# Kernel optimization log

Hardware: AMD Instinct MI355X
Metric: run time of the kernel (lower is better)

## Reference

```python
import jax, jax.numpy as jnp
import numpy as np

N = 100000   # nodes
E = 1600000  # edges (before self loops)
IN, HID, OUT = 128, 128, 64


def setup_inputs() -> dict:
    key = jax.random.key(0)
    ks = jax.random.split(key, 5)
    x = jax.random.normal(ks[0], (N, IN), dtype=jnp.float32)
    edge_index = jax.random.randint(ks[1], (2, E), 0, N, dtype=jnp.int32)
    W1 = jax.random.normal(ks[2], (IN, HID), dtype=jnp.float32) * (1.0 / np.sqrt(IN))
    b1 = jnp.zeros((HID,), dtype=jnp.float32)
    W2 = jax.random.normal(ks[3], (HID, OUT), dtype=jnp.float32) * (1.0 / np.sqrt(HID))
    b2 = jnp.zeros((OUT,), dtype=jnp.float32)
    return {"x": x, "edge_index": edge_index, "W1": W1, "b1": b1, "W2": W2, "b2": b2}


def _gcn_conv(x, W, b, src, dst, norm):
    # linear transform first (small GEMM), then normalized scatter-add aggregation
    h = x @ W                                   # [N, d_out]
    msg = h[src] * norm[:, None]                # [E+N, d_out] gathered messages
    agg = jax.ops.segment_sum(msg, dst, num_segments=N)
    return agg + b


def reference(x, edge_index, W1, b1, W2, b2):
    loops = jnp.arange(N, dtype=edge_index.dtype)
    src = jnp.concatenate([edge_index[0], loops])   # add self loops (PyG GCNConv default)
    dst = jnp.concatenate([edge_index[1], loops])
    # symmetric normalization D^{-1/2} (A+I) D^{-1/2}
    deg = jax.ops.segment_sum(jnp.ones_like(dst, dtype=x.dtype), dst, num_segments=N)
    dinv = jnp.where(deg > 0, jax.lax.rsqrt(deg), 0.0)
    norm = dinv[src] * dinv[dst]                # [E+N]

    h = _gcn_conv(x, W1, b1, src, dst, norm)
    h = jax.nn.relu(h)
    out = _gcn_conv(h, W2, b2, src, dst, norm)
    return out
```

## Files before the change

kernel.cpp:

```cpp
#include <hip/hip_runtime.h>
#include <hip/hip_bf16.h>

#define IN_DIM  128
#define HID_DIM 128
#define OUT_DIM 64

typedef unsigned short ushort_t;
struct ushort4_t { ushort_t x, y, z, w; };
typedef __attribute__((ext_vector_type(8))) short bf16x8;
typedef __attribute__((ext_vector_type(4))) float f32x4;

__device__ __forceinline__ float bf2f(ushort_t u) {
    return __uint_as_float(((unsigned int)u) << 16);
}
__device__ __forceinline__ short f2bf_s(float v) {
    __hip_bfloat16 t = __float2bfloat16(v);
    return *(short*)&t;
}
__device__ __forceinline__ unsigned int pack2(float a, float b) {
    return ((unsigned int)(ushort_t)f2bf_s(b) << 16) | (ushort_t)f2bf_s(a);
}

__global__ void count_rank(const int* __restrict__ dst, int E,
                           int* __restrict__ cnt, int* __restrict__ rank) {
    int e = blockIdx.x * blockDim.x + threadIdx.x;
    if (e < E) rank[e] = atomicAdd(&cnt[dst[e]], 1);
}

__global__ void make_dinv(const int* __restrict__ cnt, float* __restrict__ dinv, int N) {
    int i = blockIdx.x * blockDim.x + threadIdx.x;
    if (i < N) dinv[i] = rsqrtf((float)(cnt[i] + 1));
}

__global__ void scan_partial(const int* __restrict__ cnt, int* __restrict__ bsum, int N) {
    __shared__ int wsum[4];
    const int t = threadIdx.x;
    const int base = blockIdx.x * 2048 + t * 8;
    int s = 0;
    #pragma unroll
    for (int i = 0; i < 8; ++i) s += (base + i < N) ? ((cnt[base + i] + 3) & ~3) : 0;
    #pragma unroll
    for (int off = 32; off > 0; off >>= 1) s += __shfl_down(s, off);
    const int lane = t & 63, w = t >> 6;
    if (lane == 0) wsum[w] = s;
    __syncthreads();
    if (t == 0) bsum[blockIdx.x] = wsum[0] + wsum[1] + wsum[2] + wsum[3];
}

__global__ void scan_partials(int* __restrict__ bsum, int S) {
    const int t = threadIdx.x;
    int running = 0;
    for (int base = 0; base < S; base += 64) {
        int i = base + t;
        int v = (i < S) ? bsum[i] : 0;
        int incl = v;
        #pragma unroll
        for (int off = 1; off < 64; off <<= 1) {
            int u = __shfl_up(incl, off);
            if (t >= off) incl += u;
        }
        if (i < S) bsum[i] = running + incl - v;
        running += __shfl(incl, 63);
    }
}

__global__ void scan_write(const int* __restrict__ cnt, const int* __restrict__ bsum,
                           int* __restrict__ row_start, int N) {
    __shared__ int wsum[4];
    const int t = threadIdx.x;
    const int base = blockIdx.x * 2048 + t * 8;
    int v[8];
    #pragma unroll
    for (int i = 0; i < 8; ++i) v[i] = (base + i < N) ? ((cnt[base + i] + 3) & ~3) : 0;
    int s = v[0] + v[1] + v[2] + v[3] + v[4] + v[5] + v[6] + v[7];
    const int lane = t & 63, w = t >> 6;
    int incl = s;
    #pragma unroll
    for (int off = 1; off < 64; off <<= 1) {
        int u = __shfl_up(incl, off);
        if (lane >= off) incl += u;
    }
    if (lane == 63) wsum[w] = incl;
    __syncthreads();
    int woff = 0;
    for (int i = 0; i < w; ++i) woff += wsum[i];
    int run = bsum[blockIdx.x] + woff + (incl - s);
    #pragma unroll
    for (int i = 0; i < 8; ++i) {
        if (base + i < N) row_start[base + i] = run;
        run += v[i];
    }
}

__global__ void fill_pack(const int* __restrict__ src, const int* __restrict__ dst,
                          const int* __restrict__ rank, const int* __restrict__ row_start,
                          const float* __restrict__ dinv, int E, int2* __restrict__ pack) {
    int e = blockIdx.x * blockDim.x + threadIdx.x;
    if (e < E) {
        int s = src[e], d = dst[e];
        int2 p;
        p.x = s;
        p.y = __float_as_int(dinv[s] * dinv[d]);
        pack[row_start[d] + rank[e]] = p;
    }
}

__global__ __launch_bounds__(256, 2) void gemm1_mfma(
        const float* __restrict__ x, const float* __restrict__ W,
        unsigned int* __restrict__ h, int N, int NT, int NW) {
    const int tid  = threadIdx.x;
    const int lane = tid & 63;
    const int m    = lane & 15;
    const int quad = lane >> 4;
    const int gw   = blockIdx.x * 4 + (tid >> 6);

    bf16x8 a[8][4];
    #pragma unroll
    for (int ct = 0; ct < 8; ++ct)
        #pragma unroll
        for (int kc = 0; kc < 4; ++kc)
            #pragma unroll
            for (int j = 0; j < 8; ++j)
                a[ct][kc][j] = f2bf_s(W[(size_t)(kc * 32 + quad * 8 + j) * HID_DIM + ct * 16 + m]);

    for (int t = gw; t < NT; t += NW) {
        const int n0 = t * 16;
        int node = n0 + m; if (node >= N) node = N - 1;
        const float* xr = x + (size_t)node * IN_DIM + quad * 8;
        f32x4 acc[8];
        #pragma unroll
        for (int ct = 0; ct < 8; ++ct) acc[ct] = (f32x4){0.f, 0.f, 0.f, 0.f};
        #pragma unroll
        for (int kc = 0; kc < 4; ++kc) {
            const float4 v0 = *(const float4*)(xr + kc * 32);
            const float4 v1 = *(const float4*)(xr + kc * 32 + 4);
            bf16x8 b;
            b[0] = f2bf_s(v0.x); b[1] = f2bf_s(v0.y); b[2] = f2bf_s(v0.z); b[3] = f2bf_s(v0.w);
            b[4] = f2bf_s(v1.x); b[5] = f2bf_s(v1.y); b[6] = f2bf_s(v1.z); b[7] = f2bf_s(v1.w);
            #pragma unroll
            for (int ct = 0; ct < 8; ++ct)
                acc[ct] = __builtin_amdgcn_mfma_f32_16x16x32_bf16(a[ct][kc], b, acc[ct], 0, 0, 0);
        }
        if (n0 + m < N) {
            unsigned int* o = h + (size_t)(n0 + m) * (HID_DIM / 2) + quad * 2;
            #pragma unroll
            for (int ct = 0; ct < 8; ++ct) {
                uint2 pv;
                pv.x = pack2(acc[ct][0], acc[ct][1]);
                pv.y = pack2(acc[ct][2], acc[ct][3]);
                *(uint2*)(o + ct * 8) = pv;
            }
        }
    }
}

__global__ __launch_bounds__(256) void gemm2_mfma(
        const ushort_t* __restrict__ agg, const float* __restrict__ b1,
        const float* __restrict__ W2, unsigned int* __restrict__ h2,
        int N, int NT, int NW) {
    const int tid  = threadIdx.x;
    const int lane = tid & 63;
    const int m    = lane & 15;
    const int quad = lane >> 4;
    const int gw   = blockIdx.x * 4 + (tid >> 6);

    bf16x8 a[4][4];
    #pragma unroll
    for (int ct = 0; ct < 4; ++ct)
        #pragma unroll
        for (int kc = 0; kc < 4; ++kc)
            #pragma unroll
            for (int j = 0; j < 8; ++j)
                a[ct][kc][j] = f2bf_s(W2[(size_t)(kc * 32 + quad * 8 + j) * OUT_DIM + ct * 16 + m]);

    float4 b1v[8];
    #pragma unroll
    for (int kc = 0; kc < 4; ++kc) {
        b1v[kc * 2]     = *(const float4*)(b1 + kc * 32 + quad * 8);
        b1v[kc * 2 + 1] = *(const float4*)(b1 + kc * 32 + quad * 8 + 4);
    }

    for (int t = gw; t < NT; t += NW) {
        const int n0 = t * 16;
        int node = n0 + m; if (node >= N) node = N - 1;
        const ushort_t* ar = agg + (size_t)node * HID_DIM + quad * 8;
        f32x4 acc[4];
        #pragma unroll
        for (int ct = 0; ct < 4; ++ct) acc[ct] = (f32x4){0.f, 0.f, 0.f, 0.f};
        #pragma unroll
        for (int kc = 0; kc < 4; ++kc) {
            const ushort4_t r0 = *(const ushort4_t*)(ar + kc * 32);
            const ushort4_t r1 = *(const ushort4_t*)(ar + kc * 32 + 4);
            const float4 ba = b1v[kc * 2], bb = b1v[kc * 2 + 1];
            bf16x8 b;
            b[0] = f2bf_s(fmaxf(bf2f(r0.x) + ba.x, 0.f));
            b[1] = f2bf_s(fmaxf(bf2f(r0.y) + ba.y, 0.f));
            b[2] = f2bf_s(fmaxf(bf2f(r0.z) + ba.z, 0.f));
            b[3] = f2bf_s(fmaxf(bf2f(r0.w) + ba.w, 0.f));
            b[4] = f2bf_s(fmaxf(bf2f(r1.x) + bb.x, 0.f));
            b[5] = f2bf_s(fmaxf(bf2f(r1.y) + bb.y, 0.f));
            b[6] = f2bf_s(fmaxf(bf2f(r1.z) + bb.z, 0.f));
            b[7] = f2bf_s(fmaxf(bf2f(r1.w) + bb.w, 0.f));
            #pragma unroll
            for (int ct = 0; ct < 4; ++ct)
                acc[ct] = __builtin_amdgcn_mfma_f32_16x16x32_bf16(a[ct][kc], b, acc[ct], 0, 0, 0);
        }
        if (n0 + m < N) {
            unsigned int* o = h2 + (size_t)(n0 + m) * (OUT_DIM / 2) + quad * 2;
            #pragma unroll
            for (int ct = 0; ct < 4; ++ct) {
                uint2 pv;
                pv.x = pack2(acc[ct][0], acc[ct][1]);
                pv.y = pack2(acc[ct][2], acc[ct][3]);
                *(uint2*)(o + ct * 8) = pv;
            }
        }
    }
}

template<int D, bool BF16_OUT>
__global__ void gather_bf16(const ushort_t* __restrict__ h, const int2* __restrict__ pack,
                            const int* __restrict__ row_start, const int* __restrict__ cnt,
                            const float* __restrict__ dinv, const float* __restrict__ bias,
                            int N, void* __restrict__ outv) {
    const int TPN = D / 4;
    const int NPB = 256 / TPN;
    const int t = threadIdx.x;
    const int node = blockIdx.x * NPB + t / TPN;
    if (node >= N) return;
    const int f = (t & (TPN - 1)) * 4;
    const float dd = dinv[node];

    const ushort4_t self = *(const ushort4_t*)(h + (size_t)node * D + f);
    const float sn = dd * dd;
    float4 acc;
    acc.x = bf2f(self.x) * sn; acc.y = bf2f(self.y) * sn;
    acc.z = bf2f(self.z) * sn; acc.w = bf2f(self.w) * sn;
    if (bias) {
        const float4 b = *(const float4*)(bias + f);
        acc.x += b.x; acc.y += b.y; acc.z += b.z; acc.w += b.w;
    }

    const int2* pk = pack + row_start[node];
    const int cpad = (cnt[node] + 3) & ~3;
    for (int e = 0; e < cpad; e += 4) {
        const int4 a = *(const int4*)(pk + e);
        const int4 b = *(const int4*)(pk + e + 2);
        {
            const ushort4_t v = *(const ushort4_t*)(h + (size_t)a.x * D + f);
            const float n = __int_as_float(a.y);
            acc.x += bf2f(v.x) * n; acc.y += bf2f(v.y) * n;
            acc.z += bf2f(v.z) * n; acc.w += bf2f(v.w) * n;
        }
        {
            const ushort4_t v = *(const ushort4_t*)(h + (size_t)a.z * D + f);
            const float n = __int_as_float(a.w);
            acc.x += bf2f(v.x) * n; acc.y += bf2f(v.y) * n;
            acc.z += bf2f(v.z) * n; acc.w += bf2f(v.w) * n;
        }
        {
            const ushort4_t v = *(const ushort4_t*)(h + (size_t)b.x * D + f);
            const float n = __int_as_float(b.y);
            acc.x += bf2f(v.x) * n; acc.y += bf2f(v.y) * n;
            acc.z += bf2f(v.z) * n; acc.w += bf2f(v.w) * n;
        }
        {
            const ushort4_t v = *(const ushort4_t*)(h + (size_t)b.z * D + f);
            const float n = __int_as_float(b.w);
            acc.x += bf2f(v.x) * n; acc.y += bf2f(v.y) * n;
            acc.z += bf2f(v.z) * n; acc.w += bf2f(v.w) * n;
        }
    }
    if (BF16_OUT) {
        unsigned int* out = (unsigned int*)outv;
        uint2 pv;
        pv.x = pack2(acc.x, acc.y);
        pv.y = pack2(acc.z, acc.w);
        *(uint2*)(out + ((size_t)node * D + f) / 2) = pv;
    } else {
        float* out = (float*)outv;
        *(float4*)(out + (size_t)node * D + f) = acc;
    }
}

extern "C" void kernel_launch(void* const* d_in, const int* in_sizes, int n_in,
                              void* d_out, int out_size, void* d_ws, size_t ws_size,
                              hipStream_t stream) {
    const float* x   = (const float*)d_in[0];
    const int*   ei  = (const int*)  d_in[1];
    const float* W1  = (const float*)d_in[2];
    const float* b1  = (const float*)d_in[3];
    const float* W2  = (const float*)d_in[4];
    const float* b2  = (const float*)d_in[5];
    float* out = (float*)d_out;

    const int N = in_sizes[0] / IN_DIM;
    const int E = in_sizes[1] / 2;
    const int* src = ei;
    const int* dst = ei + E;

    const int PACK_CAP = E + 4 * N;
    float* dinv      = (float*)d_ws;
    int*   cnt       = (int*)(dinv + N);
    int*   row_start = cnt + N;
    int*   bsum      = row_start + N;
    size_t off       = (size_t)(3 * N + 1024);
    off = (off + 3) & ~(size_t)3;
    int2*  pack      = (int2*)((int*)d_ws + off);
    unsigned int* h1 = (unsigned int*)(pack + PACK_CAP);
    unsigned int* agg1 = h1 + (size_t)N * (HID_DIM / 2);
    int*   rank      = (int*)agg1;
    unsigned int* h2 = h1;

    const int B = 256;
    const int S = (N + 2047) / 2048;
    const int NT = (N + 15) / 16;

    hipMemsetAsync(cnt, 0, (size_t)N * sizeof(int), stream);
    hipMemsetAsync(pack, 0, (size_t)PACK_CAP * sizeof(int2), stream);
    count_rank<<<(E + B - 1) / B, B, 0, stream>>>(dst, E, cnt, rank);
    make_dinv<<<(N + B - 1) / B, B, 0, stream>>>(cnt, dinv, N);
    scan_partial<<<S, 256, 0, stream>>>(cnt, bsum, N);
    scan_partials<<<1, 64, 0, stream>>>(bsum, S);
    scan_write<<<S, 256, 0, stream>>>(cnt, bsum, row_start, N);
    fill_pack<<<(E + B - 1) / B, B, 0, stream>>>(src, dst, rank, row_start, dinv, E, pack);

    gemm1_mfma<<<512, 256, 0, stream>>>(x, W1, h1, N, NT, 512 * 4);

    gather_bf16<HID_DIM, true><<<(N + 7) / 8, 256, 0, stream>>>(
        (const ushort_t*)h1, pack, row_start, cnt, dinv, nullptr, N, (void*)agg1);

    gemm2_mfma<<<768, 256, 0, stream>>>(
        (const ushort_t*)agg1, b1, W2, h2, N, NT, 768 * 4);

    gather_bf16<OUT_DIM, false><<<(N + 15) / 16, 256, 0, stream>>>(
        (const ushort_t*)h2, pack, row_start, cnt, dinv, b2, N, (void*)out);
}
```

Measured before the change: 339.7 us.

## Replicate degree counters, merge dinv/scan pass, fuse pack fill with GEMM1

Degree counting now spreads atomics over 8 replicated counter arrays chosen by edge block, which reduces same-address atomic contention. A new node_totals kernel turns the replicas into per-replica offsets and also computes dinv, padded counts and block sums, replacing make_dinv and scan_partial. The CSR pack fill is merged into the first GEMM launch as extra blocks so the two run concurrently, and GEMM1 gets 1024 persistent blocks. In exchange the memset grows to 8N ints and fill reads one more per-edge index.

Result: slower. 363.3 us (+7.0%).

```diff
diff --git a/kernel.cpp b/kernel.cpp
--- a/kernel.cpp
+++ b/kernel.cpp
@@ -4,6 +4,8 @@
 #define IN_DIM  128
 #define HID_DIM 128
 #define OUT_DIM 64
+#define NREP    8
+#define G1B     1024
 
 typedef unsigned short ushort_t;
 struct ushort4_t { ushort_t x, y, z, w; };
@@ -21,28 +23,42 @@
     return ((unsigned int)(ushort_t)f2bf_s(b) << 16) | (ushort_t)f2bf_s(a);
 }
 
-__global__ void count_rank(const int* __restrict__ dst, int E,
-                           int* __restrict__ cnt, int* __restrict__ rank) {
+__global__ void count_rank(const int* __restrict__ dst, int E, int N,
+                           int* __restrict__ cntR, int* __restrict__ rank) {
     int e = blockIdx.x * blockDim.x + threadIdx.x;
-    if (e < E) rank[e] = atomicAdd(&cnt[dst[e]], 1);
-}
-
-__global__ void make_dinv(const int* __restrict__ cnt, float* __restrict__ dinv, int N) {
-    int i = blockIdx.x * blockDim.x + threadIdx.x;
-    if (i < N) dinv[i] = rsqrtf((float)(cnt[i] + 1));
-}
-
-__global__ void scan_partial(const int* __restrict__ cnt, int* __restrict__ bsum, int N) {
+    if (e < E) {
+        int r = (e >> 8) & (NREP - 1);
+        rank[e] = atomicAdd(&cntR[(size_t)r * N + dst[e]], 1);
+    }
+}
+
+__global__ void node_totals(int* __restrict__ cntR, float* __restrict__ dinv,
+                            int* __restrict__ cntp, int* __restrict__ bsum, int N) {
     __shared__ int wsum[4];
     const int t = threadIdx.x;
     const int base = blockIdx.x * 2048 + t * 8;
-    int s = 0;
-    #pragma unroll
-    for (int i = 0; i < 8; ++i) s += (base + i < N) ? ((cnt[base + i] + 3) & ~3) : 0;
-    #pragma unroll
-    for (int off = 32; off > 0; off >>= 1) s += __shfl_down(s, off);
+    int ssum = 0;
+    #pragma unroll
+    for (int i = 0; i < 8; ++i) {
+        const int idx = base + i;
+        if (idx < N) {
+            int b = 0;
+            #pragma unroll
+            for (int r = 0; r < NREP; ++r) {
+                int c = cntR[(size_t)r * N + idx];
+                cntR[(size_t)r * N + idx] = b;
+                b += c;
+            }
+            dinv[idx] = rsqrtf((float)(b + 1));
+            int p = (b + 3) & ~3;
+            cntp[idx] = p;
+            ssum += p;
+        }
+    }
+    #pragma unroll
+    for (int off = 32; off > 0; off >>= 1) ssum += __shfl_down(ssum, off);
     const int lane = t & 63, w = t >> 6;
-    if (lane == 0) wsum[w] = s;
+    if (lane == 0) wsum[w] = ssum;
     __syncthreads();
     if (t == 0) bsum[blockIdx.x] = wsum[0] + wsum[1] + wsum[2] + wsum[3];
 }
@@ -64,14 +80,14 @@
     }
 }
 
-__global__ void scan_write(const int* __restrict__ cnt, const int* __restrict__ bsum,
+__global__ void scan_write(const int* __restrict__ cntp, const int* __restrict__ bsum,
                            int* __restrict__ row_start, int N) {
     __shared__ int wsum[4];
     const int t = threadIdx.x;
     const int base = blockIdx.x * 2048 + t * 8;
     int v[8];
     #pragma unroll
-    for (int i = 0; i < 8; ++i) v[i] = (base + i < N) ? ((cnt[base + i] + 3) & ~3) : 0;
+    for (int i = 0; i < 8; ++i) v[i] = (base + i < N) ? cntp[base + i] : 0;
     int s = v[0] + v[1] + v[2] + v[3] + v[4] + v[5] + v[6] + v[7];
     const int lane = t & 63, w = t >> 6;
     int incl = s;
@@ -92,64 +108,69 @@
     }
 }
 
-__global__ void fill_pack(const int* __restrict__ src, const int* __restrict__ dst,
-                          const int* __restrict__ rank, const int* __restrict__ row_start,
-                          const float* __restrict__ dinv, int E, int2* __restrict__ pack) {
-    int e = blockIdx.x * blockDim.x + threadIdx.x;
-    if (e < E) {
-        int s = src[e], d = dst[e];
-        int2 p;
-        p.x = s;
-        p.y = __float_as_int(dinv[s] * dinv[d]);
-        pack[row_start[d] + rank[e]] = p;
-    }
-}
-
-__global__ __launch_bounds__(256, 2) void gemm1_mfma(
+__global__ __launch_bounds__(256, 2) void fused_fill_gemm1(
+        const int* __restrict__ src, const int* __restrict__ dst,
+        const int* __restrict__ rank, const int* __restrict__ row_start,
+        const int* __restrict__ cntR, const float* __restrict__ dinv,
+        int2* __restrict__ pack, int E,
         const float* __restrict__ x, const float* __restrict__ W,
-        unsigned int* __restrict__ h, int N, int NT, int NW) {
-    const int tid  = threadIdx.x;
-    const int lane = tid & 63;
-    const int m    = lane & 15;
-    const int quad = lane >> 4;
-    const int gw   = blockIdx.x * 4 + (tid >> 6);
-
-    bf16x8 a[8][4];
-    #pragma unroll
-    for (int ct = 0; ct < 8; ++ct)
-        #pragma unroll
-        for (int kc = 0; kc < 4; ++kc)
-            #pragma unroll
-            for (int j = 0; j < 8; ++j)
-                a[ct][kc][j] = f2bf_s(W[(size_t)(kc * 32 + quad * 8 + j) * HID_DIM + ct * 16 + m]);
-
-    for (int t = gw; t < NT; t += NW) {
-        const int n0 = t * 16;
-        int node = n0 + m; if (node >= N) node = N - 1;
-        const float* xr = x + (size_t)node * IN_DIM + quad * 8;
-        f32x4 acc[8];
-        #pragma unroll
-        for (int ct = 0; ct < 8; ++ct) acc[ct] = (f32x4){0.f, 0.f, 0.f, 0.f};
-        #pragma unroll
-        for (int kc = 0; kc < 4; ++kc) {
-            const float4 v0 = *(const float4*)(xr + kc * 32);
-            const float4 v1 = *(const float4*)(xr + kc * 32 + 4);
-            bf16x8 b;
-            b[0] = f2bf_s(v0.x); b[1] = f2bf_s(v0.y); b[2] = f2bf_s(v0.z); b[3] = f2bf_s(v0.w);
-            b[4] = f2bf_s(v1.x); b[5] = f2bf_s(v1.y); b[6] = f2bf_s(v1.z); b[7] = f2bf_s(v1.w);
-            #pragma unroll
-            for (int ct = 0; ct < 8; ++ct)
-                acc[ct] = __builtin_amdgcn_mfma_f32_16x16x32_bf16(a[ct][kc], b, acc[ct], 0, 0, 0);
-        }
-        if (n0 + m < N) {
-            unsigned int* o = h + (size_t)(n0 + m) * (HID_DIM / 2) + quad * 2;
-            #pragma unroll
-            for (int ct = 0; ct < 8; ++ct) {
-                uint2 pv;
-                pv.x = pack2(acc[ct][0], acc[ct][1]);
-                pv.y = pack2(acc[ct][2], acc[ct][3]);
-                *(uint2*)(o + ct * 8) = pv;
+        unsigned int* __restrict__ h, int N, int NT) {
+    const int tid = threadIdx.x;
+    if (blockIdx.x < G1B) {
+        const int lane = tid & 63;
+        const int m    = lane & 15;
+        const int quad = lane >> 4;
+        const int gw   = blockIdx.x * 4 + (tid >> 6);
+        const int NW   = G1B * 4;
+
+        bf16x8 a[8][4];
+        #pragma unroll
+        for (int ct = 0; ct < 8; ++ct)
+            #pragma unroll
+            for (int kc = 0; kc < 4; ++kc)
+                #pragma unroll
+                for (int j = 0; j < 8; ++j)
+                    a[ct][kc][j] = f2bf_s(W[(size_t)(kc * 32 + quad * 8 + j) * HID_DIM + ct * 16 + m]);
+
+        for (int t = gw; t < NT; t += NW) {
+            const int n0 = t * 16;
+            int node = n0 + m; if (node >= N) node = N - 1;
+            const float* xr = x + (size_t)node * IN_DIM + quad * 8;
+            f32x4 acc[8];
+            #pragma unroll
+            for (int ct = 0; ct < 8; ++ct) acc[ct] = (f32x4){0.f, 0.f, 0.f, 0.f};
+            #pragma unroll
+            for (int kc = 0; kc < 4; ++kc) {
+                const float4 v0 = *(const float4*)(xr + kc * 32);
+                const float4 v1 = *(const float4*)(xr + kc * 32 + 4);
+                bf16x8 b;
+                b[0] = f2bf_s(v0.x); b[1] = f2bf_s(v0.y); b[2] = f2bf_s(v0.z); b[3] = f2bf_s(v0.w);
+                b[4] = f2bf_s(v1.x); b[5] = f2bf_s(v1.y); b[6] = f2bf_s(v1.z); b[7] = f2bf_s(v1.w);
+                #pragma unroll
+                for (int ct = 0; ct < 8; ++ct)
+                    acc[ct] = __builtin_amdgcn_mfma_f32_16x16x32_bf16(a[ct][kc], b, acc[ct], 0, 0, 0);
             }
+            if (n0 + m < N) {
+                unsigned int* o = h + (size_t)(n0 + m) * (HID_DIM / 2) + quad * 2;
+                #pragma unroll
+                for (int ct = 0; ct < 8; ++ct) {
+                    uint2 pv;
+                    pv.x = pack2(acc[ct][0], acc[ct][1]);
+                    pv.y = pack2(acc[ct][2], acc[ct][3]);
+                    *(uint2*)(o + ct * 8) = pv;
+                }
+            }
+        }
+    } else {
+        int e = (blockIdx.x - G1B) * 256 + tid;
+        if (e < E) {
+            int s = src[e], d = dst[e];
+            int r = (e >> 8) & (NREP - 1);
+            int pos = row_start[d] + cntR[(size_t)r * N + d] + rank[e];
+            int2 p;
+            p.x = s;
+            p.y = __float_as_int(dinv[s] * dinv[d]);
+            pack[pos] = p;
         }
     }
 }
@@ -220,7 +241,7 @@
 
 template<int D, bool BF16_OUT>
 __global__ void gather_bf16(const ushort_t* __restrict__ h, const int2* __restrict__ pack,
-                            const int* __restrict__ row_start, const int* __restrict__ cnt,
+                            const int* __restrict__ row_start, const int* __restrict__ cntp,
                             const float* __restrict__ dinv, const float* __restrict__ bias,
                             int N, void* __restrict__ outv) {
     const int TPN = D / 4;
@@ -242,7 +263,7 @@
     }
 
     const int2* pk = pack + row_start[node];
-    const int cpad = (cnt[node] + 3) & ~3;
+    const int cpad = cntp[node];
     for (int e = 0; e < cpad; e += 4) {
         const int4 a = *(const int4*)(pk + e);
         const int4 b = *(const int4*)(pk + e + 2);
@@ -301,10 +322,11 @@
 
     const int PACK_CAP = E + 4 * N;
     float* dinv      = (float*)d_ws;
-    int*   cnt       = (int*)(dinv + N);
-    int*   row_start = cnt + N;
+    int*   cntp      = (int*)(dinv + N);
+    int*   row_start = cntp + N;
     int*   bsum      = row_start + N;
-    size_t off       = (size_t)(3 * N + 1024);
+    int*   cntR      = bsum + 1024;
+    size_t off       = (size_t)(3 * N + 1024 + NREP * N);
     off = (off + 3) & ~(size_t)3;
     int2*  pack      = (int2*)((int*)d_ws + off);
     unsigned int* h1 = (unsigned int*)(pack + PACK_CAP);
@@ -316,23 +338,26 @@
     const int S = (N + 2047) / 2048;
     const int NT = (N + 15) / 16;
 
-    hipMemsetAsync(cnt, 0, (size_t)N * sizeof(int), stream);
+    hipMemsetAsync(cntR, 0, (size_t)NREP * N * sizeof(int), stream);
     hipMemsetAsync(pack, 0, (size_t)PACK_CAP * sizeof(int2), stream);
-    count_rank<<<(E + B - 1) / B, B, 0, stream>>>(dst, E, cnt, rank);
-    make_dinv<<<(N + B - 1) / B, B, 0, stream>>>(cnt, dinv, N);
-    scan_partial<<<S, 256, 0, stream>>>(cnt, bsum, N);
+    count_rank<<<(E + B - 1) / B, B, 0, stream>>>(dst, E, N, cntR, rank);
+    node_totals<<<S, 256, 0, stream>>>(cntR, dinv, cntp, bsum, N);
     scan_partials<<<1, 64, 0, stream>>>(bsum, S);
-    scan_write<<<S, 256, 0, stream>>>(cnt, bsum, row_start, N);
-    fill_pack<<<(E + B - 1) / B, B, 0, stream>>>(src, dst, rank, row_start, dinv, E, pack);
-
-    gemm1_mfma<<<512, 256, 0, stream>>>(x, W1, h1, N, NT, 512 * 4);
+    scan_write<<<S, 256, 0, stream>>>(cntp, bsum, row_start, N);
+
+    {
+        int fillBlocks = (E + 255) / 256;
+        fused_fill_gemm1<<<G1B + fillBlocks, 256, 0, stream>>>(
+            src, dst, rank, row_start, cntR, dinv, pack, E,
+            x, W1, h1, N, NT);
+    }
 
     gather_bf16<HID_DIM, true><<<(N + 7) / 8, 256, 0, stream>>>(
-        (const ushort_t*)h1, pack, row_start, cnt, dinv, nullptr, N, (void*)agg1);
+        (const ushort_t*)h1, pack, row_start, cntp, dinv, nullptr, N, (void*)agg1);
 
     gemm2_mfma<<<768, 256, 0, stream>>>(
         (const ushort_t*)agg1, b1, W2, h2, N, NT, 768 * 4);
 
     gather_bf16<OUT_DIM, false><<<(N + 15) / 16, 256, 0, stream>>>(
-        (const ushort_t*)h2, pack, row_start, cnt, dinv, b2, N, (void*)out);
-}
+        (const ushort_t*)h2, pack, row_start, cntp, dinv, b2, N, (void*)out);
+}
```
